# Kernel optimization log

Measured on AMD Instinct MI355X. Metric: run time of the kernel, lower is better.

Reference implementation:

```python
import jax, jax.numpy as jnp
import numpy as np

B, S, D = 4, 2048, 1024
DFF = 512
E = 16
TOP_K = 2
N_SHARED = 2
FUSED_DFF = DFF * N_SHARED


def setup_inputs() -> dict:
    key = jax.random.key(0)
    ks = jax.random.split(key, 16)
    sc_d = 1.0 / np.sqrt(D)
    sc_f = 1.0 / np.sqrt(DFF)
    sc_sf = 1.0 / np.sqrt(FUSED_DFF)
    inp = {
        "x": jax.random.normal(ks[0], (B, S, D), dtype=jnp.float32),
        "gate_w": jax.random.uniform(ks[1], (E, D), dtype=jnp.float32, minval=-sc_d, maxval=sc_d),
        "expert_bias": jnp.zeros((E,), dtype=jnp.float32),
        # routed experts (SwiGLU): w1,w3: [E, DFF, D], w2: [E, D, DFF]
        "w1": jax.random.uniform(ks[2], (E, DFF, D), dtype=jnp.float32, minval=-sc_d, maxval=sc_d),
        "b1": jax.random.uniform(ks[3], (E, DFF), dtype=jnp.float32, minval=-sc_d, maxval=sc_d),
        "w3": jax.random.uniform(ks[4], (E, DFF, D), dtype=jnp.float32, minval=-sc_d, maxval=sc_d),
        "b3": jax.random.uniform(ks[5], (E, DFF), dtype=jnp.float32, minval=-sc_d, maxval=sc_d),
        "w2": jax.random.uniform(ks[6], (E, D, DFF), dtype=jnp.float32, minval=-sc_f, maxval=sc_f),
        "b2": jax.random.uniform(ks[7], (E, D), dtype=jnp.float32, minval=-sc_f, maxval=sc_f),
        # fused shared experts: d_model -> 2*d_ff -> d_model
        "sw1": jax.random.uniform(ks[8], (FUSED_DFF, D), dtype=jnp.float32, minval=-sc_d, maxval=sc_d),
        "sb1": jax.random.uniform(ks[9], (FUSED_DFF,), dtype=jnp.float32, minval=-sc_d, maxval=sc_d),
        "sw3": jax.random.uniform(ks[10], (FUSED_DFF, D), dtype=jnp.float32, minval=-sc_d, maxval=sc_d),
        "sb3": jax.random.uniform(ks[11], (FUSED_DFF,), dtype=jnp.float32, minval=-sc_d, maxval=sc_d),
        "sw2": jax.random.uniform(ks[12], (D, FUSED_DFF), dtype=jnp.float32, minval=-sc_sf, maxval=sc_sf),
        "sb2": jax.random.uniform(ks[13], (D,), dtype=jnp.float32, minval=-sc_sf, maxval=sc_sf),
    }
    return inp


def reference(x, gate_w, expert_bias, w1, b1, w2, b2, w3, b3,
              sw1, sb1, sw2, sb2, sw3, sb3):
    Bv, Sv, Dv = x.shape
    xf = x.reshape(-1, Dv)                                  # [T, D]
    # --- Gate (sigmoid scores, top-k over bias-adjusted logits) ---
    logits = xf @ gate_w.T                                  # [T, E]
    scores = jax.nn.sigmoid(logits)
    biased = logits + expert_bias.astype(logits.dtype)[None, :]
    _, topk_idx = jax.lax.top_k(biased, TOP_K)              # [T, K]
    topk_w = jnp.take_along_axis(scores, topk_idx, axis=-1) # [T, K]
    topk_w = topk_w / (topk_w.sum(-1, keepdims=True) + 1e-10)
    # dense per-token per-expert combine weight (zero for unselected) [T, E]
    gatew = (jax.nn.one_hot(topk_idx, E, dtype=xf.dtype) * topk_w[..., None]).sum(1)
    # --- Routed experts: equivalent to sort/dispatch/grouped-GEMM/combine ---
    y = jnp.zeros_like(xf)
    for e in range(E):
        h = jax.nn.silu(xf @ w1[e].T + b1[e]) * (xf @ w3[e].T + b3[e])  # [T, DFF]
        y = y + gatew[:, e:e + 1] * (h @ w2[e].T + b2[e])
    # --- Fused shared experts ---
    hs = jax.nn.silu(xf @ sw1.T + sb1) * (xf @ sw3.T + sb3)             # [T, 2*DFF]
    y = y + hs @ sw2.T + sb2
    return y.reshape(Bv, Sv, Dv)
```

## Files before the change

kernel.cpp:

```cpp
#include <hip/hip_runtime.h>
#include <cstdint>
#include <cstddef>

#define DEV static __device__ __forceinline__

constexpr int TT   = 8192;
constexpr int DD   = 1024;
constexpr int DFF  = 512;
constexpr int NE   = 16;
constexpr int FDFF = 1024;
constexpr int NSLOT = TT * 2;
constexpr int NSLOT_PAD = NSLOT + NE * 128;
constexpr int MAXT = NSLOT / 128 + NE;
constexpr int HB   = 64;

constexpr int RB1 = MAXT * (DFF / 64);
constexpr int SB1 = (TT / 128) * (FDFF / 64);
constexpr int NB1 = RB1 + SB1;
constexpr int NB_RG2 = MAXT * (DD / 128);
constexpr int NB_SG2 = (TT / 128) * (DD / 128);

constexpr size_t XB_OFF   = 0;
constexpr size_t HS_OFF   = XB_OFF  + (size_t)TT * DD * 2;
constexpr size_t HR_OFF   = HS_OFF  + (size_t)TT * FDFF * 2;
constexpr size_t YR_OFF   = HR_OFF  + (size_t)NSLOT_PAD * DFF * 2;
constexpr size_t W1B_OFF  = YR_OFF  + (size_t)NSLOT_PAD * DD * 2;
constexpr size_t W3B_OFF  = W1B_OFF + (size_t)NE * DFF * DD * 2;
constexpr size_t W2B_OFF  = W3B_OFF + (size_t)NE * DFF * DD * 2;
constexpr size_t SW1B_OFF = W2B_OFF + (size_t)NE * DD * DFF * 2;
constexpr size_t SW3B_OFF = SW1B_OFF + (size_t)FDFF * DD * 2;
constexpr size_t SW2B_OFF = SW3B_OFF + (size_t)FDFF * DD * 2;
constexpr size_t TKI_OFF  = SW2B_OFF + (size_t)DD * FDFF * 2;
constexpr size_t TKW_OFF  = TKI_OFF + (size_t)NSLOT * 4;
constexpr size_t STOK_OFF = TKW_OFF + (size_t)NSLOT * 4;
constexpr size_t TSL_OFF  = STOK_OFF + (size_t)NSLOT_PAD * 4;
constexpr size_t LRK_OFF  = TSL_OFF + (size_t)NSLOT * 4;
constexpr size_t BCN_OFF  = LRK_OFF + (size_t)NSLOT * 4;
constexpr size_t BB_OFF   = BCN_OFF + (size_t)HB * NE * 4;
constexpr size_t OFS_OFF  = BB_OFF + (size_t)HB * NE * 4;
constexpr size_t TEX_OFF  = OFS_OFF + 128;
constexpr size_t TM0_OFF  = TEX_OFF + (size_t)MAXT * 4;

typedef __bf16 bf16x8 __attribute__((ext_vector_type(8)));
typedef float  floatx4 __attribute__((ext_vector_type(4)));
typedef unsigned short u16t;

DEV unsigned f2bf2(float lo, float hi) {
    unsigned a = __builtin_bit_cast(unsigned, lo);
    unsigned b = __builtin_bit_cast(unsigned, hi);
    a += 0x7FFFu + ((a >> 16) & 1u);
    b += 0x7FFFu + ((b >> 16) & 1u);
    return (a >> 16) | (b & 0xFFFF0000u);
}
DEV u16t f2bf1(float f) {
    unsigned u = __builtin_bit_cast(unsigned, f);
    u += 0x7FFFu + ((u >> 16) & 1u);
    return (u16t)(u >> 16);
}
DEV float bf2f(u16t v) {
    return __builtin_bit_cast(float, ((unsigned)v) << 16);
}
DEV uint4 pack8(float4 a, float4 b) {
    uint4 r;
    r.x = f2bf2(a.x, a.y); r.y = f2bf2(a.z, a.w);
    r.z = f2bf2(b.x, b.y); r.w = f2bf2(b.z, b.w);
    return r;
}
DEV floatx4 mfma16(bf16x8 a, bf16x8 b, floatx4 c) {
    return __builtin_amdgcn_mfma_f32_16x16x32_bf16(a, b, c, 0, 0, 0);
}
DEV void glds16(const u16t* g, u16t* l) {
    __builtin_amdgcn_global_load_lds(
        (const __attribute__((address_space(1))) unsigned int*)g,
        (__attribute__((address_space(3))) unsigned int*)l, 16, 0, 0);
}
DEV float dot4(float4 a, float4 b) { return a.x*b.x + a.y*b.y + a.z*b.z + a.w*b.w; }

__global__ __launch_bounds__(256) void k_cvtw(
        const float* __restrict__ w1, const float* __restrict__ w3, const float* __restrict__ w2,
        const float* __restrict__ sw1, const float* __restrict__ sw3, const float* __restrict__ sw2,
        u16t* __restrict__ w1b, u16t* __restrict__ w3b, u16t* __restrict__ w2b,
        u16t* __restrict__ sw1b, u16t* __restrict__ sw3b, u16t* __restrict__ sw2b) {
    int b = blockIdx.x;
    const float* src; u16t* dst; size_t base;
    if      (b < 4096)  { src = w1;  dst = w1b;  base = (size_t)b * 2048; }
    else if (b < 8192)  { src = w3;  dst = w3b;  base = (size_t)(b - 4096) * 2048; }
    else if (b < 12288) { src = w2;  dst = w2b;  base = (size_t)(b - 8192) * 2048; }
    else if (b < 12800) { src = sw1; dst = sw1b; base = (size_t)(b - 12288) * 2048; }
    else if (b < 13312) { src = sw3; dst = sw3b; base = (size_t)(b - 12800) * 2048; }
    else                { src = sw2; dst = sw2b; base = (size_t)(b - 13312) * 2048; }
    size_t i = base + (size_t)threadIdx.x * 8;
    float4 a = *(const float4*)(src + i);
    float4 c = *(const float4*)(src + i + 4);
    *(uint4*)(dst + i) = pack8(a, c);
}

__global__ __launch_bounds__(256) void k_gate(const float* __restrict__ x,
                                              const float* __restrict__ gw,
                                              const float* __restrict__ eb,
                                              int* __restrict__ tki, float* __restrict__ tkw,
                                              u16t* __restrict__ xb) {
    const int tid = threadIdx.x;
    const int wave = tid >> 6, lane = tid & 63;
    const int tok0 = blockIdx.x * 16 + wave * 4;
    float acc[4][16];
#pragma unroll
    for (int t = 0; t < 4; t++)
#pragma unroll
        for (int e = 0; e < 16; e++) acc[t][e] = 0.f;
#pragma unroll
    for (int i = 0; i < 4; i++) {
        const int d = i * 256 + lane * 4;
        float4 xv[4];
#pragma unroll
        for (int t = 0; t < 4; t++) xv[t] = *(const float4*)(x + (size_t)(tok0 + t) * DD + d);
#pragma unroll
        for (int t = 0; t < 4; t++) {
            uint2 p;
            p.x = f2bf2(xv[t].x, xv[t].y);
            p.y = f2bf2(xv[t].z, xv[t].w);
            *(uint2*)(xb + (size_t)(tok0 + t) * DD + d) = p;
        }
#pragma unroll
        for (int e = 0; e < 16; e++) {
            float4 wv = *(const float4*)(gw + (size_t)e * DD + d);
#pragma unroll
            for (int t = 0; t < 4; t++) acc[t][e] += dot4(xv[t], wv);
        }
    }
#pragma unroll
    for (int t = 0; t < 4; t++)
#pragma unroll
        for (int e = 0; e < 16; e++) {
            float v = acc[t][e];
            v += __shfl_xor(v, 1);  v += __shfl_xor(v, 2);  v += __shfl_xor(v, 4);
            v += __shfl_xor(v, 8);  v += __shfl_xor(v, 16); v += __shfl_xor(v, 32);
            acc[t][e] = v;
        }
    if (lane == 0) {
        float ebs[16];
#pragma unroll
        for (int e = 0; e < 16; e++) ebs[e] = eb[e];
#pragma unroll
        for (int t = 0; t < 4; t++) {
            float b0 = -1e30f, b1v = -1e30f, l0 = 0.f, l1 = 0.f;
            int i0 = 0, i1 = 0;
#pragma unroll
            for (int e = 0; e < 16; e++) {
                float lv = acc[t][e];
                float bl = lv + ebs[e];
                if (bl > b0)       { b1v = b0; i1 = i0; l1 = l0; b0 = bl; i0 = e; l0 = lv; }
                else if (bl > b1v) { b1v = bl; i1 = e; l1 = lv; }
            }
            float s0 = 1.f / (1.f + expf(-l0));
            float s1 = 1.f / (1.f + expf(-l1));
            float dn = s0 + s1 + 1e-10f;
            int tok = tok0 + t;
            tki[tok * 2] = i0; tki[tok * 2 + 1] = i1;
            tkw[tok * 2] = s0 / dn; tkw[tok * 2 + 1] = s1 / dn;
        }
    }
}

__global__ __launch_bounds__(256) void k_hist(const int* __restrict__ tki,
                                              int* __restrict__ lrank, int* __restrict__ bcnt) {
    __shared__ int h[NE];
    const int tid = threadIdx.x;
    if (tid < NE) h[tid] = 0;
    __syncthreads();
    int idx = blockIdx.x * 256 + tid;
    int e = tki[idx];
    lrank[idx] = atomicAdd(&h[e], 1);
    __syncthreads();
    if (tid < NE) bcnt[blockIdx.x * NE + tid] = h[tid];
}

__global__ void k_scan(const int* __restrict__ bcnt, int* __restrict__ offs,
                       int* __restrict__ bb, int* __restrict__ texp, int* __restrict__ tm0) {
    __shared__ int cntS[NE], offS[NE];
    const int tid = threadIdx.x;
    if (tid < NE) {
        int s = 0;
#pragma unroll
        for (int b = 0; b < HB; b++) s += bcnt[b * NE + tid];
        cntS[tid] = s;
    }
    __syncthreads();
    if (tid == 0) {
        int off = 0, t = 0;
        for (int e = 0; e < NE; e++) {
            offS[e] = off; offs[e] = off;
            int nt = (cntS[e] + 127) >> 7;
            for (int i = 0; i < nt; i++) { texp[t] = e; tm0[t] = off + i * 128; t++; }
            off += nt * 128;
        }
        offs[NE] = off;
        for (; t < MAXT; t++) texp[t] = -1;
    }
    __syncthreads();
    if (tid < NE) {
        int run = offS[tid];
        for (int b = 0; b < HB; b++) { bb[b * NE + tid] = run; run += bcnt[b * NE + tid]; }
    }
}

__global__ __launch_bounds__(256) void k_scatter(const int* __restrict__ tki,
                                                 const int* __restrict__ bb,
                                                 const int* __restrict__ lrank,
                                                 int* __restrict__ stok,
                                                 int* __restrict__ tslot) {
    int idx = blockIdx.x * 256 + threadIdx.x;
    int e = tki[idx];
    int slot = bb[blockIdx.x * NE + e] + lrank[idx];
    stok[slot] = idx >> 1;
    tslot[idx] = slot;
}

__global__ __launch_bounds__(256) void k_gemm1(const u16t* __restrict__ xb,
        const u16t* __restrict__ w1b, const float* __restrict__ b1,
        const u16t* __restrict__ w3b, const float* __restrict__ b3,
        const u16t* __restrict__ sw1b, const float* __restrict__ sb1,
        const u16t* __restrict__ sw3b, const float* __restrict__ sb3,
        const int* __restrict__ stok,
        const int* __restrict__ texp, const int* __restrict__ tm0,
        u16t* __restrict__ Hr, u16t* __restrict__ Hs) {
    __shared__ u16t As[128 * 32], B1s[64 * 32], B3s[64 * 32];
    const int tid = threadIdx.x, lane = tid & 63, wid = tid >> 6;
    const int wm = (wid & 1) * 64, wn = (wid >> 1) * 32;
    const int q = lane >> 4, r = lane & 15;
    const int srow = tid >> 2, scg = (tid & 3) * 8;

    const int swz = ((int)blockIdx.x & 7) * (NB1 / 8) + ((int)blockIdx.x >> 3);
    const u16t *a0, *a1, *bg1, *bg3;
    const float *bs1, *bs3;
    u16t* hout; int m0, n0, ostr;
    if (swz < RB1) {
        const int mt = swz >> 3, nb = swz & 7;
        const int te = texp[mt];
        if (te < 0) return;
        m0 = tm0[mt]; n0 = nb * 64;
        int t0 = stok[m0 + srow];      if (t0 < 0) t0 = 0;
        int t1 = stok[m0 + 64 + srow]; if (t1 < 0) t1 = 0;
        a0 = xb + (size_t)t0 * DD + scg;
        a1 = xb + (size_t)t1 * DD + scg;
        bg1 = w1b + (size_t)te * DFF * DD + (size_t)(n0 + srow) * DD + scg;
        bg3 = w3b + (size_t)te * DFF * DD + (size_t)(n0 + srow) * DD + scg;
        bs1 = b1 + (size_t)te * DFF;
        bs3 = b3 + (size_t)te * DFF;
        hout = Hr; ostr = DFF;
    } else {
        const int s = swz - RB1;
        const int mt = s >> 4, nb = s & 15;
        m0 = mt * 128; n0 = nb * 64;
        a0 = xb + (size_t)(m0 + srow) * DD + scg;
        a1 = xb + (size_t)(m0 + 64 + srow) * DD + scg;
        bg1 = sw1b + (size_t)(n0 + srow) * DD + scg;
        bg3 = sw3b + (size_t)(n0 + srow) * DD + scg;
        bs1 = sb1; bs3 = sb3;
        hout = Hs; ostr = FDFF;
    }

    floatx4 acc1[4][2], acc3[4][2];
#pragma unroll
    for (int i = 0; i < 4; i++)
#pragma unroll
        for (int j = 0; j < 2; j++) { acc1[i][j] = (floatx4)0.f; acc3[i][j] = (floatx4)0.f; }
    u16t* lA0 = As + tid * 8;
    u16t* lA1 = As + 2048 + tid * 8;
    u16t* lB1 = B1s + tid * 8;
    u16t* lB3 = B3s + tid * 8;
    for (int k0 = 0; k0 < DD; k0 += 32) {
        glds16(a0 + k0, lA0); glds16(a1 + k0, lA1);
        glds16(bg1 + k0, lB1); glds16(bg3 + k0, lB3);
        __syncthreads();
        bf16x8 af[4], f1[2], f3[2];
#pragma unroll
        for (int i = 0; i < 4; i++) af[i] = *(const bf16x8*)&As[(wm + i * 16 + r) * 32 + q * 8];
#pragma unroll
        for (int j = 0; j < 2; j++) {
            f1[j] = *(const bf16x8*)&B1s[(wn + j * 16 + r) * 32 + q * 8];
            f3[j] = *(const bf16x8*)&B3s[(wn + j * 16 + r) * 32 + q * 8];
        }
#pragma unroll
        for (int i = 0; i < 4; i++)
#pragma unroll
            for (int j = 0; j < 2; j++) {
                acc1[i][j] = mfma16(af[i], f1[j], acc1[i][j]);
                acc3[i][j] = mfma16(af[i], f3[j], acc3[i][j]);
            }
        __syncthreads();
    }
    float s1v[2], s3v[2];
#pragma unroll
    for (int j = 0; j < 2; j++) {
        int col = n0 + wn + j * 16 + r;
        s1v[j] = bs1[col]; s3v[j] = bs3[col];
    }
#pragma unroll
    for (int i = 0; i < 4; i++)
#pragma unroll
        for (int j = 0; j < 2; j++)
#pragma unroll
            for (int g = 0; g < 4; g++) {
                int row = m0 + wm + i * 16 + q * 4 + g;
                int col = n0 + wn + j * 16 + r;
                float z1 = acc1[i][j][g] + s1v[j];
                float z3 = acc3[i][j][g] + s3v[j];
                float h = (z1 / (1.f + __expf(-z1))) * z3;
                hout[(size_t)row * ostr + col] = f2bf1(h);
            }
}

__global__ __launch_bounds__(256) void k_rgemm2(const u16t* __restrict__ Hr,
        const u16t* __restrict__ w2b, const float* __restrict__ b2,
        const int* __restrict__ texp, const int* __restrict__ tm0,
        u16t* __restrict__ Yr) {
    const int swz = ((int)blockIdx.x & 7) * (NB_RG2 / 8) + ((int)blockIdx.x >> 3);
    const int mt = swz >> 3, nb = swz & 7;
    const int te = texp[mt];
    if (te < 0) return;
    const int m0 = tm0[mt], n0 = nb * 128;
    __shared__ u16t As[128 * 32], Bs[128 * 32];
    const int tid = threadIdx.x, lane = tid & 63, wid = tid >> 6;
    const int wm = (wid & 1) * 64, wn = (wid >> 1) * 64;
    const int q = lane >> 4, r = lane & 15;
    const int srow = tid >> 2, scg = (tid & 3) * 8;
    floatx4 acc[4][4];
#pragma unroll
    for (int i = 0; i < 4; i++)
#pragma unroll
        for (int j = 0; j < 4; j++) acc[i][j] = (floatx4)0.f;
    const u16t* a0 = Hr + (size_t)(m0 + srow) * DFF + scg;
    const u16t* a1 = Hr + (size_t)(m0 + 64 + srow) * DFF + scg;
    const u16t* b0 = w2b + (size_t)te * DD * DFF + (size_t)(n0 + srow) * DFF + scg;
    const u16t* b1 = w2b + (size_t)te * DD * DFF + (size_t)(n0 + 64 + srow) * DFF + scg;
    const float* b2e = b2 + (size_t)te * DD;
    u16t* lA0 = As + tid * 8;       u16t* lA1 = As + 2048 + tid * 8;
    u16t* lB0 = Bs + tid * 8;       u16t* lB1 = Bs + 2048 + tid * 8;
    for (int k0 = 0; k0 < DFF; k0 += 32) {
        glds16(a0 + k0, lA0); glds16(a1 + k0, lA1);
        glds16(b0 + k0, lB0); glds16(b1 + k0, lB1);
        __syncthreads();
        bf16x8 af[4], bf[4];
#pragma unroll
        for (int i = 0; i < 4; i++) af[i] = *(const bf16x8*)&As[(wm + i * 16 + r) * 32 + q * 8];
#pragma unroll
        for (int j = 0; j < 4; j++) bf[j] = *(const bf16x8*)&Bs[(wn + j * 16 + r) * 32 + q * 8];
#pragma unroll
        for (int i = 0; i < 4; i++)
#pragma unroll
            for (int j = 0; j < 4; j++) acc[i][j] = mfma16(af[i], bf[j], acc[i][j]);
        __syncthreads();
    }
    float bv[4];
#pragma unroll
    for (int j = 0; j < 4; j++) bv[j] = b2e[n0 + wn + j * 16 + r];
#pragma unroll
    for (int i = 0; i < 4; i++)
#pragma unroll
        for (int g = 0; g < 4; g++) {
            int slot = m0 + wm + i * 16 + q * 4 + g;
#pragma unroll
            for (int j = 0; j < 4; j++) {
                int col = n0 + wn + j * 16 + r;
                Yr[(size_t)slot * DD + col] = f2bf1(acc[i][j][g] + bv[j]);
            }
        }
}

__global__ __launch_bounds__(256) void k_sgemm2(const u16t* __restrict__ Hs,
        const u16t* __restrict__ sw2b, const float* __restrict__ sb2,
        const u16t* __restrict__ Yr, const int* __restrict__ tslot,
        const float* __restrict__ tkw,
        float* __restrict__ out) {
    const int swz = ((int)blockIdx.x & 7) * (NB_SG2 / 8) + ((int)blockIdx.x >> 3);
    const int mt = swz >> 3, nb = swz & 7;
    const int m0 = mt * 128, n0 = nb * 128;
    __shared__ u16t As[128 * 32], Bs[128 * 32];
    __shared__ int sl[256];
    __shared__ float wl[256];
    const int tid = threadIdx.x, lane = tid & 63, wid = tid >> 6;
    const int wm = (wid & 1) * 64, wn = (wid >> 1) * 64;
    const int q = lane >> 4, r = lane & 15;
    const int srow = tid >> 2, scg = (tid & 3) * 8;
    sl[tid] = tslot[m0 * 2 + tid];
    wl[tid] = tkw[m0 * 2 + tid];
    floatx4 acc[4][4];
#pragma unroll
    for (int i = 0; i < 4; i++)
#pragma unroll
        for (int j = 0; j < 4; j++) acc[i][j] = (floatx4)0.f;
    const u16t* a0 = Hs + (size_t)(m0 + srow) * FDFF + scg;
    const u16t* a1 = Hs + (size_t)(m0 + 64 + srow) * FDFF + scg;
    const u16t* b0 = sw2b + (size_t)(n0 + srow) * FDFF + scg;
    const u16t* b1 = sw2b + (size_t)(n0 + 64 + srow) * FDFF + scg;
    u16t* lA0 = As + tid * 8;       u16t* lA1 = As + 2048 + tid * 8;
    u16t* lB0 = Bs + tid * 8;       u16t* lB1 = Bs + 2048 + tid * 8;
    for (int k0 = 0; k0 < FDFF; k0 += 32) {
        glds16(a0 + k0, lA0); glds16(a1 + k0, lA1);
        glds16(b0 + k0, lB0); glds16(b1 + k0, lB1);
        __syncthreads();
        bf16x8 af[4], bf[4];
#pragma unroll
        for (int i = 0; i < 4; i++) af[i] = *(const bf16x8*)&As[(wm + i * 16 + r) * 32 + q * 8];
#pragma unroll
        for (int j = 0; j < 4; j++) bf[j] = *(const bf16x8*)&Bs[(wn + j * 16 + r) * 32 + q * 8];
#pragma unroll
        for (int i = 0; i < 4; i++)
#pragma unroll
            for (int j = 0; j < 4; j++) acc[i][j] = mfma16(af[i], bf[j], acc[i][j]);
        __syncthreads();
    }
    float bv[4];
#pragma unroll
    for (int j = 0; j < 4; j++) bv[j] = sb2[n0 + wn + j * 16 + r];
#pragma unroll
    for (int i = 0; i < 4; i++)
#pragma unroll
        for (int g = 0; g < 4; g++) {
            int rowl = wm + i * 16 + q * 4 + g;
            int s0 = sl[rowl * 2], s1 = sl[rowl * 2 + 1];
            float w0 = wl[rowl * 2], w1 = wl[rowl * 2 + 1];
            const u16t* y0p = Yr + (size_t)s0 * DD;
            const u16t* y1p = Yr + (size_t)s1 * DD;
#pragma unroll
            for (int j = 0; j < 4; j++) {
                int col = n0 + wn + j * 16 + r;
                float v = acc[i][j][g] + bv[j];
                v += w0 * bf2f(y0p[col]) + w1 * bf2f(y1p[col]);
                out[(size_t)(m0 + rowl) * DD + col] = v;
            }
        }
}

extern "C" void kernel_launch(void* const* d_in, const int* in_sizes, int n_in,
                              void* d_out, int out_size, void* d_ws, size_t ws_size,
                              hipStream_t stream) {
    const float* x   = (const float*)d_in[0];
    const float* gw  = (const float*)d_in[1];
    const float* eb  = (const float*)d_in[2];
    const float* w1  = (const float*)d_in[3];
    const float* b1  = (const float*)d_in[4];
    const float* w3  = (const float*)d_in[5];
    const float* b3  = (const float*)d_in[6];
    const float* w2  = (const float*)d_in[7];
    const float* b2  = (const float*)d_in[8];
    const float* sw1 = (const float*)d_in[9];
    const float* sb1 = (const float*)d_in[10];
    const float* sw3 = (const float*)d_in[11];
    const float* sb3 = (const float*)d_in[12];
    const float* sw2 = (const float*)d_in[13];
    const float* sb2 = (const float*)d_in[14];
    float* out = (float*)d_out;
    char* ws = (char*)d_ws;

    u16t*  xb   = (u16t*)(ws + XB_OFF);
    u16t*  Hs   = (u16t*)(ws + HS_OFF);
    u16t*  Hr   = (u16t*)(ws + HR_OFF);
    u16t*  Yr   = (u16t*)(ws + YR_OFF);
    u16t*  w1b  = (u16t*)(ws + W1B_OFF);
    u16t*  w3b  = (u16t*)(ws + W3B_OFF);
    u16t*  w2b  = (u16t*)(ws + W2B_OFF);
    u16t*  sw1b = (u16t*)(ws + SW1B_OFF);
    u16t*  sw3b = (u16t*)(ws + SW3B_OFF);
    u16t*  sw2b = (u16t*)(ws + SW2B_OFF);
    int*   tki  = (int*)(ws + TKI_OFF);
    float* tkw  = (float*)(ws + TKW_OFF);
    int*   stok = (int*)(ws + STOK_OFF);
    int*   tslot = (int*)(ws + TSL_OFF);
    int*   lrank = (int*)(ws + LRK_OFF);
    int*   bcnt = (int*)(ws + BCN_OFF);
    int*   bb   = (int*)(ws + BB_OFF);
    int*   offs = (int*)(ws + OFS_OFF);
    int*   texp = (int*)(ws + TEX_OFF);
    int*   tm0  = (int*)(ws + TM0_OFF);

    hipMemsetAsync(stok, 0xFF, (size_t)NSLOT_PAD * 4, stream);

    k_cvtw<<<13824, 256, 0, stream>>>(w1, w3, w2, sw1, sw3, sw2, w1b, w3b, w2b, sw1b, sw3b, sw2b);
    k_gate<<<512, 256, 0, stream>>>(x, gw, eb, tki, tkw, xb);
    k_hist<<<HB, 256, 0, stream>>>(tki, lrank, bcnt);
    k_scan<<<1, 64, 0, stream>>>(bcnt, offs, bb, texp, tm0);
    k_scatter<<<HB, 256, 0, stream>>>(tki, bb, lrank, stok, tslot);

    k_gemm1<<<NB1, 256, 0, stream>>>(xb, w1b, b1, w3b, b3, sw1b, sb1, sw3b, sb3,
                                     stok, texp, tm0, Hr, Hs);
    k_rgemm2<<<NB_RG2, 256, 0, stream>>>(Hr, w2b, b2, texp, tm0, Yr);
    k_sgemm2<<<NB_SG2, 256, 0, stream>>>(Hs, sw2b, sb2, Yr, tslot, tkw, out);
}
```

Measured before the change: 385.9 us.

## Double GEMM K-tile to 64 and XOR-swizzle LDS layout in all three GEMMs

In all three MFMA GEMM kernels the K step per iteration grows from 32 to 64, so each block stages 128x64 and 64/128x64 tiles per barrier pair. The LDS layout gets an XOR swizzle on the 8-element column chunks, which is meant to avoid bank conflicts on the 128-byte row stride. The goal is to halve the number of __syncthreads and load-issue rounds per K and cut LDS conflicts. The cost is double the LDS per block, which may lower occupancy, and there is still no double buffering.

```diff
diff --git a/kernel.cpp b/kernel.cpp
--- a/kernel.cpp
+++ b/kernel.cpp
@@ -76,6 +76,7 @@
 }
 DEV float dot4(float4 a, float4 b) { return a.x*b.x + a.y*b.y + a.z*b.z + a.w*b.w; }
 
+
 __global__ __launch_bounds__(256) void k_cvtw(
         const float* __restrict__ w1, const float* __restrict__ w3, const float* __restrict__ w2,
         const float* __restrict__ sw1, const float* __restrict__ sw3, const float* __restrict__ sw2,
@@ -224,14 +225,17 @@
         const int* __restrict__ stok,
         const int* __restrict__ texp, const int* __restrict__ tm0,
         u16t* __restrict__ Hr, u16t* __restrict__ Hs) {
-    __shared__ u16t As[128 * 32], B1s[64 * 32], B3s[64 * 32];
+    __shared__ u16t As[128 * 64], B1s[64 * 64], B3s[64 * 64];
     const int tid = threadIdx.x, lane = tid & 63, wid = tid >> 6;
     const int wm = (wid & 1) * 64, wn = (wid >> 1) * 32;
     const int q = lane >> 4, r = lane & 15;
-    const int srow = tid >> 2, scg = (tid & 3) * 8;
+    const int srow8 = tid >> 3;
+    const int scg8 = (((tid & 7) ^ ((tid >> 3) & 7)) * 8);
+    const int rc0 = ((q) ^ (r & 7)) * 8;
+    const int rc1 = ((4 + q) ^ (r & 7)) * 8;
 
     const int swz = ((int)blockIdx.x & 7) * (NB1 / 8) + ((int)blockIdx.x >> 3);
-    const u16t *a0, *a1, *bg1, *bg3;
+    const u16t *a0, *a1, *a2, *a3, *bg1a, *bg1b, *bg3a, *bg3b;
     const float *bs1, *bs3;
     u16t* hout; int m0, n0, ostr;
     if (swz < RB1) {
@@ -239,12 +243,20 @@
         const int te = texp[mt];
         if (te < 0) return;
         m0 = tm0[mt]; n0 = nb * 64;
-        int t0 = stok[m0 + srow];      if (t0 < 0) t0 = 0;
-        int t1 = stok[m0 + 64 + srow]; if (t1 < 0) t1 = 0;
-        a0 = xb + (size_t)t0 * DD + scg;
-        a1 = xb + (size_t)t1 * DD + scg;
-        bg1 = w1b + (size_t)te * DFF * DD + (size_t)(n0 + srow) * DD + scg;
-        bg3 = w3b + (size_t)te * DFF * DD + (size_t)(n0 + srow) * DD + scg;
+        int t0 = stok[m0 + srow8];       if (t0 < 0) t0 = 0;
+        int t1 = stok[m0 + 32 + srow8];  if (t1 < 0) t1 = 0;
+        int t2 = stok[m0 + 64 + srow8];  if (t2 < 0) t2 = 0;
+        int t3 = stok[m0 + 96 + srow8];  if (t3 < 0) t3 = 0;
+        a0 = xb + (size_t)t0 * DD + scg8;
+        a1 = xb + (size_t)t1 * DD + scg8;
+        a2 = xb + (size_t)t2 * DD + scg8;
+        a3 = xb + (size_t)t3 * DD + scg8;
+        const u16t* wb1 = w1b + (size_t)te * DFF * DD;
+        const u16t* wb3 = w3b + (size_t)te * DFF * DD;
+        bg1a = wb1 + (size_t)(n0 + srow8) * DD + scg8;
+        bg1b = wb1 + (size_t)(n0 + 32 + srow8) * DD + scg8;
+        bg3a = wb3 + (size_t)(n0 + srow8) * DD + scg8;
+        bg3b = wb3 + (size_t)(n0 + 32 + srow8) * DD + scg8;
         bs1 = b1 + (size_t)te * DFF;
         bs3 = b3 + (size_t)te * DFF;
         hout = Hr; ostr = DFF;
@@ -252,10 +264,14 @@
         const int s = swz - RB1;
         const int mt = s >> 4, nb = s & 15;
         m0 = mt * 128; n0 = nb * 64;
-        a0 = xb + (size_t)(m0 + srow) * DD + scg;
-        a1 = xb + (size_t)(m0 + 64 + srow) * DD + scg;
-        bg1 = sw1b + (size_t)(n0 + srow) * DD + scg;
-        bg3 = sw3b + (size_t)(n0 + srow) * DD + scg;
+        a0 = xb + (size_t)(m0 + srow8) * DD + scg8;
+        a1 = xb + (size_t)(m0 + 32 + srow8) * DD + scg8;
+        a2 = xb + (size_t)(m0 + 64 + srow8) * DD + scg8;
+        a3 = xb + (size_t)(m0 + 96 + srow8) * DD + scg8;
+        bg1a = sw1b + (size_t)(n0 + srow8) * DD + scg8;
+        bg1b = sw1b + (size_t)(n0 + 32 + srow8) * DD + scg8;
+        bg3a = sw3b + (size_t)(n0 + srow8) * DD + scg8;
+        bg3b = sw3b + (size_t)(n0 + 32 + srow8) * DD + scg8;
         bs1 = sb1; bs3 = sb3;
         hout = Hs; ostr = FDFF;
     }
@@ -265,29 +281,51 @@
     for (int i = 0; i < 4; i++)
 #pragma unroll
         for (int j = 0; j < 2; j++) { acc1[i][j] = (floatx4)0.f; acc3[i][j] = (floatx4)0.f; }
-    u16t* lA0 = As + tid * 8;
-    u16t* lA1 = As + 2048 + tid * 8;
-    u16t* lB1 = B1s + tid * 8;
-    u16t* lB3 = B3s + tid * 8;
-    for (int k0 = 0; k0 < DD; k0 += 32) {
-        glds16(a0 + k0, lA0); glds16(a1 + k0, lA1);
-        glds16(bg1 + k0, lB1); glds16(bg3 + k0, lB3);
+
+    for (int k0 = 0; k0 < DD; k0 += 64) {
+        glds16(a0 + k0, As + tid * 8);
+        glds16(a1 + k0, As + 2048 + tid * 8);
+        glds16(a2 + k0, As + 4096 + tid * 8);
+        glds16(a3 + k0, As + 6144 + tid * 8);
+        glds16(bg1a + k0, B1s + tid * 8);
+        glds16(bg1b + k0, B1s + 2048 + tid * 8);
+        glds16(bg3a + k0, B3s + tid * 8);
+        glds16(bg3b + k0, B3s + 2048 + tid * 8);
         __syncthreads();
-        bf16x8 af[4], f1[2], f3[2];
-#pragma unroll
-        for (int i = 0; i < 4; i++) af[i] = *(const bf16x8*)&As[(wm + i * 16 + r) * 32 + q * 8];
-#pragma unroll
-        for (int j = 0; j < 2; j++) {
-            f1[j] = *(const bf16x8*)&B1s[(wn + j * 16 + r) * 32 + q * 8];
-            f3[j] = *(const bf16x8*)&B3s[(wn + j * 16 + r) * 32 + q * 8];
-        }
-#pragma unroll
-        for (int i = 0; i < 4; i++)
+        {
+            bf16x8 af[4], f1[2], f3[2];
+#pragma unroll
+            for (int i = 0; i < 4; i++) af[i] = *(const bf16x8*)&As[(wm + i * 16 + r) * 64 + rc0];
 #pragma unroll
             for (int j = 0; j < 2; j++) {
-                acc1[i][j] = mfma16(af[i], f1[j], acc1[i][j]);
-                acc3[i][j] = mfma16(af[i], f3[j], acc3[i][j]);
+                f1[j] = *(const bf16x8*)&B1s[(wn + j * 16 + r) * 64 + rc0];
+                f3[j] = *(const bf16x8*)&B3s[(wn + j * 16 + r) * 64 + rc0];
             }
+#pragma unroll
+            for (int i = 0; i < 4; i++)
+#pragma unroll
+                for (int j = 0; j < 2; j++) {
+                    acc1[i][j] = mfma16(af[i], f1[j], acc1[i][j]);
+                    acc3[i][j] = mfma16(af[i], f3[j], acc3[i][j]);
+                }
+        }
+        {
+            bf16x8 af[4], f1[2], f3[2];
+#pragma unroll
+            for (int i = 0; i < 4; i++) af[i] = *(const bf16x8*)&As[(wm + i * 16 + r) * 64 + rc1];
+#pragma unroll
+            for (int j = 0; j < 2; j++) {
+                f1[j] = *(const bf16x8*)&B1s[(wn + j * 16 + r) * 64 + rc1];
+                f3[j] = *(const bf16x8*)&B3s[(wn + j * 16 + r) * 64 + rc1];
+            }
+#pragma unroll
+            for (int i = 0; i < 4; i++)
+#pragma unroll
+                for (int j = 0; j < 2; j++) {
+                    acc1[i][j] = mfma16(af[i], f1[j], acc1[i][j]);
+                    acc3[i][j] = mfma16(af[i], f3[j], acc3[i][j]);
+                }
+        }
         __syncthreads();
     }
     float s1v[2], s3v[2];
@@ -320,36 +358,61 @@
     const int te = texp[mt];
     if (te < 0) return;
     const int m0 = tm0[mt], n0 = nb * 128;
-    __shared__ u16t As[128 * 32], Bs[128 * 32];
+    __shared__ u16t As[128 * 64], Bs[128 * 64];
     const int tid = threadIdx.x, lane = tid & 63, wid = tid >> 6;
     const int wm = (wid & 1) * 64, wn = (wid >> 1) * 64;
     const int q = lane >> 4, r = lane & 15;
-    const int srow = tid >> 2, scg = (tid & 3) * 8;
+    const int srow8 = tid >> 3;
+    const int scg8 = (((tid & 7) ^ ((tid >> 3) & 7)) * 8);
+    const int rc0 = ((q) ^ (r & 7)) * 8;
+    const int rc1 = ((4 + q) ^ (r & 7)) * 8;
     floatx4 acc[4][4];
 #pragma unroll
     for (int i = 0; i < 4; i++)
 #pragma unroll
         for (int j = 0; j < 4; j++) acc[i][j] = (floatx4)0.f;
-    const u16t* a0 = Hr + (size_t)(m0 + srow) * DFF + scg;
-    const u16t* a1 = Hr + (size_t)(m0 + 64 + srow) * DFF + scg;
-    const u16t* b0 = w2b + (size_t)te * DD * DFF + (size_t)(n0 + srow) * DFF + scg;
-    const u16t* b1 = w2b + (size_t)te * DD * DFF + (size_t)(n0 + 64 + srow) * DFF + scg;
+    const u16t* a0 = Hr + (size_t)(m0 + srow8) * DFF + scg8;
+    const u16t* a1 = Hr + (size_t)(m0 + 32 + srow8) * DFF + scg8;
+    const u16t* a2 = Hr + (size_t)(m0 + 64 + srow8) * DFF + scg8;
+    const u16t* a3 = Hr + (size_t)(m0 + 96 + srow8) * DFF + scg8;
+    const u16t* wbe = w2b + (size_t)te * DD * DFF;
+    const u16t* b0 = wbe + (size_t)(n0 + srow8) * DFF + scg8;
+    const u16t* b1 = wbe + (size_t)(n0 + 32 + srow8) * DFF + scg8;
+    const u16t* b2p = wbe + (size_t)(n0 + 64 + srow8) * DFF + scg8;
+    const u16t* b3p = wbe + (size_t)(n0 + 96 + srow8) * DFF + scg8;
     const float* b2e = b2 + (size_t)te * DD;
-    u16t* lA0 = As + tid * 8;       u16t* lA1 = As + 2048 + tid * 8;
-    u16t* lB0 = Bs + tid * 8;       u16t* lB1 = Bs + 2048 + tid * 8;
-    for (int k0 = 0; k0 < DFF; k0 += 32) {
-        glds16(a0 + k0, lA0); glds16(a1 + k0, lA1);
-        glds16(b0 + k0, lB0); glds16(b1 + k0, lB1);
+    for (int k0 = 0; k0 < DFF; k0 += 64) {
+        glds16(a0 + k0, As + tid * 8);
+        glds16(a1 + k0, As + 2048 + tid * 8);
+        glds16(a2 + k0, As + 4096 + tid * 8);
+        glds16(a3 + k0, As + 6144 + tid * 8);
+        glds16(b0 + k0, Bs + tid * 8);
+        glds16(b1 + k0, Bs + 2048 + tid * 8);
+        glds16(b2p + k0, Bs + 4096 + tid * 8);
+        glds16(b3p + k0, Bs + 6144 + tid * 8);
         __syncthreads();
-        bf16x8 af[4], bf[4];
-#pragma unroll
-        for (int i = 0; i < 4; i++) af[i] = *(const bf16x8*)&As[(wm + i * 16 + r) * 32 + q * 8];
-#pragma unroll
-        for (int j = 0; j < 4; j++) bf[j] = *(const bf16x8*)&Bs[(wn + j * 16 + r) * 32 + q * 8];
-#pragma unroll
-        for (int i = 0; i < 4; i++)
-#pragma unroll
-            for (int j = 0; j < 4; j++) acc[i][j] = mfma16(af[i], bf[j], acc[i][j]);
+        {
+            bf16x8 af[4], bf[4];
+#pragma unroll
+            for (int i = 0; i < 4; i++) af[i] = *(const bf16x8*)&As[(wm + i * 16 + r) * 64 + rc0];
+#pragma unroll
+            for (int j = 0; j < 4; j++) bf[j] = *(const bf16x8*)&Bs[(wn + j * 16 + r) * 64 + rc0];
+#pragma unroll
+            for (int i = 0; i < 4; i++)
+#pragma unroll
+                for (int j = 0; j < 4; j++) acc[i][j] = mfma16(af[i], bf[j], acc[i][j]);
+        }
+        {
+            bf16x8 af[4], bf[4];
+#pragma unroll
+            for (int i = 0; i < 4; i++) af[i] = *(const bf16x8*)&As[(wm + i * 16 + r) * 64 + rc1];
+#pragma unroll
+            for (int j = 0; j < 4; j++) bf[j] = *(const bf16x8*)&Bs[(wn + j * 16 + r) * 64 + rc1];
+#pragma unroll
+            for (int i = 0; i < 4; i++)
+#pragma unroll
+                for (int j = 0; j < 4; j++) acc[i][j] = mfma16(af[i], bf[j], acc[i][j]);
+        }
         __syncthreads();
     }
     float bv[4];
@@ -376,13 +439,16 @@
     const int swz = ((int)blockIdx.x & 7) * (NB_SG2 / 8) + ((int)blockIdx.x >> 3);
     const int mt = swz >> 3, nb = swz & 7;
     const int m0 = mt * 128, n0 = nb * 128;
-    __shared__ u16t As[128 * 32], Bs[128 * 32];
+    __shared__ u16t As[128 * 64], Bs[128 * 64];
     __shared__ int sl[256];
     __shared__ float wl[256];
     const int tid = threadIdx.x, lane = tid & 63, wid = tid >> 6;
     const int wm = (wid & 1) * 64, wn = (wid >> 1) * 64;
     const int q = lane >> 4, r = lane & 15;
-    const int srow = tid >> 2, scg = (tid & 3) * 8;
+    const int srow8 = tid >> 3;
+    const int scg8 = (((tid & 7) ^ ((tid >> 3) & 7)) * 8);
+    const int rc0 = ((q) ^ (r & 7)) * 8;
+    const int rc1 = ((4 + q) ^ (r & 7)) * 8;
     sl[tid] = tslot[m0 * 2 + tid];
     wl[tid] = tkw[m0 * 2 + tid];
     floatx4 acc[4][4];
@@ -390,25 +456,46 @@
     for (int i = 0; i < 4; i++)
 #pragma unroll
         for (int j = 0; j < 4; j++) acc[i][j] = (floatx4)0.f;
-    const u16t* a0 = Hs + (size_t)(m0 + srow) * FDFF + scg;
-    const u16t* a1 = Hs + (size_t)(m0 + 64 + srow) * FDFF + scg;
-    const u16t* b0 = sw2b + (size_t)(n0 + srow) * FDFF + scg;
-    const u16t* b1 = sw2b + (size_t)(n0 + 64 + srow) * FDFF + scg;
-    u16t* lA0 = As + tid * 8;       u16t* lA1 = As + 2048 + tid * 8;
-    u16t* lB0 = Bs + tid * 8;       u16t* lB1 = Bs + 2048 + tid * 8;
-    for (int k0 = 0; k0 < FDFF; k0 += 32) {
-        glds16(a0 + k0, lA0); glds16(a1 + k0, lA1);
-        glds16(b0 + k0, lB0); glds16(b1 + k0, lB1);
+    const u16t* a0 = Hs + (size_t)(m0 + srow8) * FDFF + scg8;
+    const u16t* a1 = Hs + (size_t)(m0 + 32 + srow8) * FDFF + scg8;
+    const u16t* a2 = Hs + (size_t)(m0 + 64 + srow8) * FDFF + scg8;
+    const u16t* a3 = Hs + (size_t)(m0 + 96 + srow8) * FDFF + scg8;
+    const u16t* b0 = sw2b + (size_t)(n0 + srow8) * FDFF + scg8;
+    const u16t* b1 = sw2b + (size_t)(n0 + 32 + srow8) * FDFF + scg8;
+    const u16t* b2p = sw2b + (size_t)(n0 + 64 + srow8) * FDFF + scg8;
+    const u16t* b3p = sw2b + (size_t)(n0 + 96 + srow8) * FDFF + scg8;
+    for (int k0 = 0; k0 < FDFF; k0 += 64) {
+        glds16(a0 + k0, As + tid * 8);
+        glds16(a1 + k0, As + 2048 + tid * 8);
+        glds16(a2 + k0, As + 4096 + tid * 8);
+        glds16(a3 + k0, As + 6144 + tid * 8);
+        glds16(b0 + k0, Bs + tid * 8);
+        glds16(b1 + k0, Bs + 2048 + tid * 8);
+        glds16(b2p + k0, Bs + 4096 + tid * 8);
+        glds16(b3p + k0, Bs + 6144 + tid * 8);
         __syncthreads();
-        bf16x8 af[4], bf[4];
-#pragma unroll
-        for (int i = 0; i < 4; i++) af[i] = *(const bf16x8*)&As[(wm + i * 16 + r) * 32 + q * 8];
-#pragma unroll
-        for (int j = 0; j < 4; j++) bf[j] = *(const bf16x8*)&Bs[(wn + j * 16 + r) * 32 + q * 8];
-#pragma unroll
-        for (int i = 0; i < 4; i++)
-#pragma unroll
-            for (int j = 0; j < 4; j++) acc[i][j] = mfma16(af[i], bf[j], acc[i][j]);
+        {
+            bf16x8 af[4], bf[4];
+#pragma unroll
+            for (int i = 0; i < 4; i++) af[i] = *(const bf16x8*)&As[(wm + i * 16 + r) * 64 + rc0];
+#pragma unroll
+            for (int j = 0; j < 4; j++) bf[j] = *(const bf16x8*)&Bs[(wn + j * 16 + r) * 64 + rc0];
+#pragma unroll
+            for (int i = 0; i < 4; i++)
+#pragma unroll
+                for (int j = 0; j < 4; j++) acc[i][j] = mfma16(af[i], bf[j], acc[i][j]);
+        }
+        {
+            bf16x8 af[4], bf[4];
+#pragma unroll
+            for (int i = 0; i < 4; i++) af[i] = *(const bf16x8*)&As[(wm + i * 16 + r) * 64 + rc1];
+#pragma unroll
+            for (int j = 0; j < 4; j++) bf[j] = *(const bf16x8*)&Bs[(wn + j * 16 + r) * 64 + rc1];
+#pragma unroll
+            for (int i = 0; i < 4; i++)
+#pragma unroll
+                for (int j = 0; j < 4; j++) acc[i][j] = mfma16(af[i], bf[j], acc[i][j]);
+        }
         __syncthreads();
     }
     float bv[4];
```

Result: no change. 392.2 us (+1.6%).
